# Performance work log

Hardware: AMD Instinct MI355X
Metric: run time of the kernel (lower is better)

## Reference

```python
import jax, jax.numpy as jnp
import numpy as np

N, D, NUM_CLASSES = 4096, 1024, 64


def setup_inputs() -> dict:
    key = jax.random.key(0)
    k1, k2 = jax.random.split(key)
    inputs = jax.random.normal(k1, (N, D), dtype=jnp.float32)
    labels = jax.random.randint(k2, (N,), 0, NUM_CLASSES, dtype=jnp.int64)
    return {"inputs": inputs, "labels": labels}


def reference(inputs, labels):
    # dist_mat = inputs @ inputs.T  (raw dot-product 'cosine_dist', no normalization)
    dist = jnp.matmul(inputs, inputs.T)  # [N, N]
    n = inputs.shape[0]
    same = labels[:, None] == labels[None, :]          # [N, N]
    eye = jnp.eye(n, dtype=bool)
    is_pos = same & ~eye                               # same label, excluding self
    is_neg = ~same                                     # different label
    # hardest-positive: +2 penalty on non-positive entries, then row argmin
    d_ap = jnp.where(is_pos, dist, dist + 2.0)
    # 'easiest' negative: +2 penalty on non-negative entries, then row argmin
    d_an = jnp.where(is_neg, dist, dist + 2.0)
    id_ap = jnp.argmin(d_ap, axis=1)                   # [N]
    id_an = jnp.argmin(d_an, axis=1)                   # [N]
    # (The original also computes a semi-hard id_an_semi, but returns id_an;
    #  that block is dead code w.r.t. the output, so it is omitted.)
    return (inputs[id_ap], inputs[id_an])
```

## Files before the change

### kernel.cpp

```cpp
#include <hip/hip_runtime.h>
#include <cstdint>

#define N 4096
#define D 1024
#define KC_COUNT (D / 32)
#define NP 4128
#define RGP (NP / 16)
#define TG (NP / 96)
#define NBLK (TG * (TG + 1) / 2)

typedef _Float16 f16;
typedef __attribute__((ext_vector_type(4))) _Float16 f16x4;
typedef __attribute__((ext_vector_type(8))) _Float16 f16x8;
typedef __attribute__((ext_vector_type(4))) float f32x4;

__device__ __forceinline__ unsigned int orderable(float f) {
    unsigned int b = __float_as_uint(f);
    return (b & 0x80000000u) ? ~b : (b | 0x80000000u);
}

__device__ __forceinline__ void async_copy16(const f16* g, f16* l) {
    __builtin_amdgcn_global_load_lds(
        (const __attribute__((address_space(1))) uint32_t*)(const void*)g,
        (__attribute__((address_space(3))) uint32_t*)(void*)l,
        16 , 0 , 0 );
}

#define KSPAN 256
#define SS_STRIDE (KSPAN + 24)
__global__ __launch_bounds__(256) void split_swizzle(
    const float* __restrict__ X, f16* __restrict__ Xsw,
    unsigned long long* __restrict__ keys)
{
    __shared__ f16 Hs[16 * SS_STRIDE];
    __shared__ f16 Ls[16 * SS_STRIDE];
    const int tid = threadIdx.x;
    const int bid = blockIdx.x;
    const int rg = bid >> 2, kq = bid & 3;
    if (bid < 32) keys[bid * 256 + tid] = 0xFFFFFFFFFFFFFFFFull;

    if (rg >= 256) {
        const uint4 z = {0, 0, 0, 0};
#pragma unroll
        for (int i = 0; i < 4; ++i) {
            const int o = i * 256 + tid;
            const int kcl = o >> 7, rem = o & 127;
            const int kc = kq * 8 + kcl;
            *(uint4*)(Xsw + (((size_t)rg * KC_COUNT + kc) * 2) * 512 + rem * 8) = z;
        }
        return;
    }

#pragma unroll
    for (int i = 0; i < 4; ++i) {
        const int idx4 = i * 256 + tid;
        const int row = idx4 >> 6, c4 = idx4 & 63;
        const float4 v = *(const float4*)(X + (size_t)(rg * 16 + row) * D + kq * KSPAN + c4 * 4);
        const float xs[4] = {v.x, v.y, v.z, v.w};
        f16x4 h, l;
#pragma unroll
        for (int e = 0; e < 4; ++e) {
            f16 hh = (f16)xs[e];
            h[e] = hh;
            l[e] = (f16)(xs[e] - (float)hh);
        }
        *(f16x4*)(Hs + row * SS_STRIDE + c4 * 4) = h;
        *(f16x4*)(Ls + row * SS_STRIDE + c4 * 4) = l;
    }
    __syncthreads();

#pragma unroll
    for (int hl = 0; hl < 2; ++hl) {
        const f16* lds = hl ? Ls : Hs;
#pragma unroll
        for (int i = 0; i < 2; ++i) {
            const int o = i * 256 + tid;
            const int kcl = o >> 6, lo_ = o & 63;
            const int q = lo_ >> 4, m = lo_ & 15;
            const uint4 v = *(const uint4*)(lds + m * SS_STRIDE + kcl * 32 + q * 8);
            const int kc = kq * 8 + kcl;
            *(uint4*)(Xsw + (((size_t)rg * KC_COUNT + kc) * 2 + hl) * 512 + lo_ * 8) = v;
        }
    }
}

__global__ __launch_bounds__(256, 4) void gemm_argmin_sym(
    const f16* __restrict__ Xsw, const int* __restrict__ labels,
    unsigned long long* __restrict__ keys_ap,
    unsigned long long* __restrict__ keys_an)
{
    __shared__ f16 As[6 * 2 * 512];
    __shared__ f16 Bs[6 * 2 * 512];

    int r = blockIdx.x, ti = 0;
    while (r >= TG - ti) { r -= TG - ti; ++ti; }
    const int tj = ti + r;

    const int tid = threadIdx.x;
    const int lane = tid & 63;
    const int w = tid >> 6;
    const int wr = w >> 1, wc = w & 1;
    const int rowBase = ti * 96, colBase = tj * 96;

    f32x4 acc[3][3];
#pragma unroll
    for (int mi = 0; mi < 3; ++mi)
#pragma unroll
        for (int ni = 0; ni < 3; ++ni) acc[mi][ni] = (f32x4){0.f, 0.f, 0.f, 0.f};

    const f16* g[6];
    f16* lp[6];
#pragma unroll
    for (int j = 0; j < 6; ++j) {
        int c = w * 6 + j;
        int isB = c >= 12, rem = isB ? c - 12 : c, rgL = rem >> 1, hl = rem & 1;
        int rgG = (isB ? tj : ti) * 6 + rgL;
        g[j] = Xsw + ((((size_t)rgG * KC_COUNT) * 2 + hl) * 64 + lane) * 8;
        lp[j] = (isB ? Bs : As) + (rgL * 2 + hl) * 512;
    }

    for (int kc = 0; kc < KC_COUNT; ++kc) {
#pragma unroll
        for (int j = 0; j < 6; ++j)
            async_copy16(g[j] + (size_t)kc * 1024, lp[j]);
        __syncthreads();

        f16x8 ah[3], al[3], bh[3], bl[3];
#pragma unroll
        for (int t2 = 0; t2 < 3; ++t2) {
            int rgA = wr * 3 + t2, rgB = wc * 3 + t2;
            ah[t2] = *(const f16x8*)(As + (rgA * 2 + 0) * 512 + lane * 8);
            al[t2] = *(const f16x8*)(As + (rgA * 2 + 1) * 512 + lane * 8);
            bh[t2] = *(const f16x8*)(Bs + (rgB * 2 + 0) * 512 + lane * 8);
            bl[t2] = *(const f16x8*)(Bs + (rgB * 2 + 1) * 512 + lane * 8);
        }
#pragma unroll
        for (int mi = 0; mi < 3; ++mi)
#pragma unroll
            for (int ni = 0; ni < 3; ++ni) {
                acc[mi][ni] = __builtin_amdgcn_mfma_f32_16x16x32_f16(
                    ah[mi], bh[ni], acc[mi][ni], 0, 0, 0);
                acc[mi][ni] = __builtin_amdgcn_mfma_f32_16x16x32_f16(
                    ah[mi], bl[ni], acc[mi][ni], 0, 0, 0);
                acc[mi][ni] = __builtin_amdgcn_mfma_f32_16x16x32_f16(
                    al[mi], bh[ni], acc[mi][ni], 0, 0, 0);
            }
        __syncthreads();
    }

    const int g16 = lane >> 4, c16 = lane & 15;

    int ljv[3], liv[3][4];
#pragma unroll
    for (int ni = 0; ni < 3; ++ni) {
        const int j = colBase + wc * 48 + ni * 16 + c16;
        ljv[ni] = (j < N) ? labels[j] : -1;
    }
#pragma unroll
    for (int mi = 0; mi < 3; ++mi)
#pragma unroll
        for (int reg = 0; reg < 4; ++reg) {
            const int i = rowBase + wr * 48 + mi * 16 + g16 * 4 + reg;
            liv[mi][reg] = (i < N) ? labels[i] : -1;
        }

#pragma unroll
    for (int mi = 0; mi < 3; ++mi) {
#pragma unroll
        for (int reg = 0; reg < 4; ++reg) {
            const int i = rowBase + wr * 48 + mi * 16 + g16 * 4 + reg;
            const int li = liv[mi][reg];
            float bestAp = __builtin_huge_valf(); int jAp = 0;
            float bestAn = __builtin_huge_valf(); int jAn = 0;
#pragma unroll
            for (int ni = 0; ni < 3; ++ni) {
                const int jcol = colBase + wc * 48 + ni * 16 + c16;
                const float v = acc[mi][ni][reg];
                const bool same = (li == ljv[ni]);
                const float vap = (same && (i != jcol)) ? v : v + 2.0f;
                const float van = (!same) ? v : v + 2.0f;
                if (vap < bestAp) { bestAp = vap; jAp = jcol; }
                if (van < bestAn) { bestAn = van; jAn = jcol; }
            }
            unsigned long long kap =
                ((unsigned long long)orderable(bestAp) << 32) | (unsigned)jAp;
            unsigned long long kan =
                ((unsigned long long)orderable(bestAn) << 32) | (unsigned)jAn;
#pragma unroll
            for (int off = 1; off < 16; off <<= 1) {
                unsigned long long o = __shfl_xor(kap, off); kap = o < kap ? o : kap;
                o = __shfl_xor(kan, off); kan = o < kan ? o : kan;
            }
            if (c16 == 0 && i < N) {
                atomicMin(&keys_ap[i], kap);
                atomicMin(&keys_an[i], kan);
            }
        }
    }

    if (ti != tj) {
#pragma unroll
        for (int ni = 0; ni < 3; ++ni) {
            const int j = colBase + wc * 48 + ni * 16 + c16;
            const int lj = ljv[ni];
            float bestAp = __builtin_huge_valf(); int iAp = 0;
            float bestAn = __builtin_huge_valf(); int iAn = 0;
#pragma unroll
            for (int mi = 0; mi < 3; ++mi)
#pragma unroll
                for (int reg = 0; reg < 4; ++reg) {
                    const int i = rowBase + wr * 48 + mi * 16 + g16 * 4 + reg;
                    const float v = acc[mi][ni][reg];
                    const bool same = (liv[mi][reg] == lj);
                    const float vap = same ? v : v + 2.0f;
                    const float van = (!same) ? v : v + 2.0f;
                    if (vap < bestAp) { bestAp = vap; iAp = i; }
                    if (van < bestAn) { bestAn = van; iAn = i; }
                }
            unsigned long long kap =
                ((unsigned long long)orderable(bestAp) << 32) | (unsigned)iAp;
            unsigned long long kan =
                ((unsigned long long)orderable(bestAn) << 32) | (unsigned)iAn;
#pragma unroll
            for (int off = 16; off < 64; off <<= 1) {
                unsigned long long o = __shfl_xor(kap, off); kap = o < kap ? o : kap;
                o = __shfl_xor(kan, off); kan = o < kan ? o : kan;
            }
            if (g16 == 0 && j < N) {
                atomicMin(&keys_ap[j], kap);
                atomicMin(&keys_an[j], kan);
            }
        }
    }
}

__global__ void gather_rows(const float* __restrict__ A,
                            const unsigned long long* __restrict__ keys_ap,
                            const unsigned long long* __restrict__ keys_an,
                            float* __restrict__ out)
{
    const int row = blockIdx.x;
    const int t = threadIdx.x;
    const int ja = (int)(keys_ap[row] & 0xFFFFFFFFull);
    const int jn = (int)(keys_an[row] & 0xFFFFFFFFull);
    const float4* Av = (const float4*)A;
    float4* Ov = (float4*)out;
    Ov[(size_t)row * (D / 4) + t]       = Av[(size_t)ja * (D / 4) + t];
    Ov[(size_t)(N + row) * (D / 4) + t] = Av[(size_t)jn * (D / 4) + t];
}

extern "C" void kernel_launch(void* const* d_in, const int* in_sizes, int n_in,
                              void* d_out, int out_size, void* d_ws, size_t ws_size,
                              hipStream_t stream) {
    const float* A = (const float*)d_in[0];
    const int* labels = (const int*)d_in[1];
    float* out = (float*)d_out;

    unsigned long long* keys = (unsigned long long*)d_ws;
    f16* Xsw = (f16*)((char*)d_ws + 65536);

    split_swizzle<<<RGP * 4, 256, 0, stream>>>(A, Xsw, keys);
    gemm_argmin_sym<<<NBLK, 256, 0, stream>>>(Xsw, labels, keys, keys + N);
    gather_rows<<<N, 256, 0, stream>>>(A, keys, keys + N, out);
}
```

Before: 155.0 us.

## Double-buffer LDS tiles and overlap async global loads with MFMA compute

Replaces the single-buffered K loop, which had a full load-then-sync per K chunk, with a two-stage LDS ping-pong pipeline. Async global-to-LDS copies for chunk k+2 are issued in slices between MFMA groups, with explicit vmcnt/lgkmcnt waits, raw barriers and s_setprio around the MFMAs. The goal is to hide global memory latency behind matrix math. In exchange LDS use doubles and launch bounds drop from 4 to 3 blocks per CU, which lowers occupancy.

```diff
diff --git a/kernel.cpp b/kernel.cpp
--- a/kernel.cpp
+++ b/kernel.cpp
@@ -84,13 +84,58 @@
     }
 }
 
-__global__ __launch_bounds__(256, 4) void gemm_argmin_sym(
+#define BUF_HALF 6144
+
+template<int STAGE, int VM>
+__device__ __forceinline__ void kstep(
+    const f16* a, const f16* b,
+    const f16* const (&g)[6], f16* const (&lp)[6],
+    size_t go, int bufoff, int wr, int wc, int lane,
+    f32x4 (&acc)[3][3])
+{
+    f16x8 ah[3], al[3], bh[3], bl[3];
+#pragma unroll
+    for (int t2 = 0; t2 < 3; ++t2) {
+        const int rgA = wr * 3 + t2, rgB = wc * 3 + t2;
+        ah[t2] = *(const f16x8*)(a + (rgA * 2 + 0) * 512 + lane * 8);
+        al[t2] = *(const f16x8*)(a + (rgA * 2 + 1) * 512 + lane * 8);
+        bh[t2] = *(const f16x8*)(b + (rgB * 2 + 0) * 512 + lane * 8);
+        bl[t2] = *(const f16x8*)(b + (rgB * 2 + 1) * 512 + lane * 8);
+    }
+    asm volatile("s_waitcnt lgkmcnt(0)" ::: "memory");
+    __builtin_amdgcn_s_barrier();
+
+#pragma unroll
+    for (int mi = 0; mi < 3; ++mi) {
+        if (STAGE) {
+            async_copy16(g[2 * mi]     + go, lp[2 * mi]     + bufoff);
+            async_copy16(g[2 * mi + 1] + go, lp[2 * mi + 1] + bufoff);
+        }
+        __builtin_amdgcn_s_setprio(1);
+#pragma unroll
+        for (int ni = 0; ni < 3; ++ni) {
+            acc[mi][ni] = __builtin_amdgcn_mfma_f32_16x16x32_f16(
+                ah[mi], bh[ni], acc[mi][ni], 0, 0, 0);
+            acc[mi][ni] = __builtin_amdgcn_mfma_f32_16x16x32_f16(
+                ah[mi], bl[ni], acc[mi][ni], 0, 0, 0);
+            acc[mi][ni] = __builtin_amdgcn_mfma_f32_16x16x32_f16(
+                al[mi], bh[ni], acc[mi][ni], 0, 0, 0);
+        }
+        __builtin_amdgcn_s_setprio(0);
+        if (mi < 2) __builtin_amdgcn_s_barrier();
+    }
+    if (VM == 6) asm volatile("s_waitcnt vmcnt(6)" ::: "memory");
+    else if (VM == 0) asm volatile("s_waitcnt vmcnt(0)" ::: "memory");
+    if (VM >= 0) __builtin_amdgcn_s_barrier();
+}
+
+__global__ __launch_bounds__(256, 3) void gemm_argmin_sym(
     const f16* __restrict__ Xsw, const int* __restrict__ labels,
     unsigned long long* __restrict__ keys_ap,
     unsigned long long* __restrict__ keys_an)
 {
-    __shared__ f16 As[6 * 2 * 512];
-    __shared__ f16 Bs[6 * 2 * 512];
+    __shared__ f16 As[2][BUF_HALF];
+    __shared__ f16 Bs[2][BUF_HALF];
 
     int r = blockIdx.x, ti = 0;
     while (r >= TG - ti) { r -= TG - ti; ++ti; }
@@ -116,37 +161,25 @@
         int isB = c >= 12, rem = isB ? c - 12 : c, rgL = rem >> 1, hl = rem & 1;
         int rgG = (isB ? tj : ti) * 6 + rgL;
         g[j] = Xsw + ((((size_t)rgG * KC_COUNT) * 2 + hl) * 64 + lane) * 8;
-        lp[j] = (isB ? Bs : As) + (rgL * 2 + hl) * 512;
-    }
-
-    for (int kc = 0; kc < KC_COUNT; ++kc) {
-#pragma unroll
-        for (int j = 0; j < 6; ++j)
-            async_copy16(g[j] + (size_t)kc * 1024, lp[j]);
-        __syncthreads();
-
-        f16x8 ah[3], al[3], bh[3], bl[3];
-#pragma unroll
-        for (int t2 = 0; t2 < 3; ++t2) {
-            int rgA = wr * 3 + t2, rgB = wc * 3 + t2;
-            ah[t2] = *(const f16x8*)(As + (rgA * 2 + 0) * 512 + lane * 8);
-            al[t2] = *(const f16x8*)(As + (rgA * 2 + 1) * 512 + lane * 8);
-            bh[t2] = *(const f16x8*)(Bs + (rgB * 2 + 0) * 512 + lane * 8);
-            bl[t2] = *(const f16x8*)(Bs + (rgB * 2 + 1) * 512 + lane * 8);
-        }
-#pragma unroll
-        for (int mi = 0; mi < 3; ++mi)
-#pragma unroll
-            for (int ni = 0; ni < 3; ++ni) {
-                acc[mi][ni] = __builtin_amdgcn_mfma_f32_16x16x32_f16(
-                    ah[mi], bh[ni], acc[mi][ni], 0, 0, 0);
-                acc[mi][ni] = __builtin_amdgcn_mfma_f32_16x16x32_f16(
-                    ah[mi], bl[ni], acc[mi][ni], 0, 0, 0);
-                acc[mi][ni] = __builtin_amdgcn_mfma_f32_16x16x32_f16(
-                    al[mi], bh[ni], acc[mi][ni], 0, 0, 0);
-            }
-        __syncthreads();
-    }
+        lp[j] = (isB ? Bs[0] : As[0]) + (rgL * 2 + hl) * 512;
+    }
+
+#pragma unroll
+    for (int j = 0; j < 6; ++j) async_copy16(g[j], lp[j]);
+#pragma unroll
+    for (int j = 0; j < 6; ++j) async_copy16(g[j] + 1024, lp[j] + BUF_HALF);
+    asm volatile("s_waitcnt vmcnt(6)" ::: "memory");
+    __builtin_amdgcn_s_barrier();
+
+#pragma unroll 1
+    for (int t = 0; t < KC_COUNT - 2; t += 2) {
+        kstep<1, 6>(As[0], Bs[0], g, lp, (size_t)(t + 2) * 1024, 0,
+                    wr, wc, lane, acc);
+        kstep<1, 6>(As[1], Bs[1], g, lp, (size_t)(t + 3) * 1024, BUF_HALF,
+                    wr, wc, lane, acc);
+    }
+    kstep<0, 0>(As[0], Bs[0], g, lp, 0, 0, wr, wc, lane, acc);
+    kstep<0, -1>(As[1], Bs[1], g, lp, 0, 0, wr, wc, lane, acc);
 
     const int g16 = lane >> 4, c16 = lane & 15;
 
```

Measured after the change: 154.2 us. No clear change (-0.5%).
